# Performance work log

Hardware: AMD Instinct MI355X
Metric: run time of the kernel (lower is better)

## Reference

```python
import jax, jax.numpy as jnp
import numpy as np

B, S, D = 2, 1024, 768      # batch, seq, d_model
F, F_UP = 8192, 8192        # downstream / upstream dictionary sizes
K = 64                      # top-k of the downstream AE
MASK_DENSITY = 0.05         # fraction of allowed feature-feature connections


def setup_inputs() -> dict:
    key = jax.random.key(0)
    ks = jax.random.split(key, 12)
    inv_sqrt_d = 1.0 / np.sqrt(D)
    resid = jax.random.normal(ks[0], (B, S, D), dtype=jnp.float32)
    # upstream pruned features: k-sparse-ish non-negative activations
    pruned0 = jax.nn.relu(jax.random.normal(ks[1], (B, S, F_UP)) - 2.0).astype(jnp.float32)
    pruned1 = jax.nn.relu(jax.random.normal(ks[2], (B, S, F_UP)) - 2.0).astype(jnp.float32)
    feature_buffer = jnp.zeros((B, S, F), dtype=jnp.float32)
    W_enc = jax.random.normal(ks[3], (F, D), dtype=jnp.float32) * inv_sqrt_d
    b_enc = jax.random.normal(ks[4], (F,), dtype=jnp.float32) * 0.01
    W_dec = jax.random.normal(ks[5], (F, D), dtype=jnp.float32) * inv_sqrt_d
    b_dec = jax.random.normal(ks[6], (D,), dtype=jnp.float32) * 0.01
    W_dec_up0 = jax.random.normal(ks[7], (F_UP, D), dtype=jnp.float32) * inv_sqrt_d
    W_dec_up1 = jax.random.normal(ks[8], (F_UP, D), dtype=jnp.float32) * inv_sqrt_d
    b_dec_up0 = jax.random.normal(ks[9], (D,), dtype=jnp.float32) * 0.01
    b_dec_up1 = jax.random.normal(ks[10], (D,), dtype=jnp.float32) * 0.01
    km0, km1 = jax.random.split(ks[11])
    mask0 = (jax.random.uniform(km0, (F, F_UP)) < MASK_DENSITY).astype(jnp.float32)
    mask1 = (jax.random.uniform(km1, (F, F_UP)) < MASK_DENSITY).astype(jnp.float32)
    return {
        "resid": resid, "pruned0": pruned0, "pruned1": pruned1,
        "feature_buffer": feature_buffer,
        "W_enc": W_enc, "b_enc": b_enc, "W_dec": W_dec, "b_dec": b_dec,
        "W_dec_up0": W_dec_up0, "W_dec_up1": W_dec_up1,
        "b_dec_up0": b_dec_up0, "b_dec_up1": b_dec_up1,
        "mask0": mask0, "mask1": mask1, "k": K,
    }


def reference(resid, pruned0, pruned1, feature_buffer,
              W_enc, b_enc, W_dec, b_dec,
              W_dec_up0, W_dec_up1, b_dec_up0, b_dec_up1,
              mask0, mask1, k):
    # initial contributions: encode the cached residual stream, [B,S,F]
    approx = jnp.einsum("bsd,fd->bsf", resid, W_enc)
    upstream_bias = b_dec_up0 + b_dec_up1
    # accumulate connection-masked upstream contributions
    for pruned, W_dec_up, mask in ((pruned0, W_dec_up0, mask0),
                                   (pruned1, W_dec_up1, mask1)):
        # masked virtual weights: [F, F_up]
        virtual = jnp.einsum("fd,ud->fu", W_enc, W_dec_up) * mask
        approx = approx + jnp.einsum("bsu,fu->bsf", pruned, virtual)
    # bias correction: project summed upstream decoder biases, add encoder bias
    approx = approx + jnp.einsum("fd,d->f", W_enc, upstream_bias) + b_enc
    # topk (unsorted set equals torch's sorted=False), relu, scatter into buffer
    top_vals, top_idx = jax.lax.top_k(approx, k)        # [B,S,k]
    top_vals = jax.nn.relu(top_vals)
    Bn, Sn, Fn = feature_buffer.shape
    bi = jnp.arange(Bn)[:, None, None]
    si = jnp.arange(Sn)[None, :, None]
    feat_buffer = jnp.zeros_like(feature_buffer).at[bi, si, top_idx].set(top_vals)
    # dense decode
    reconstructions = jnp.einsum("bsf,fd->bsd", feat_buffer, W_dec) + b_dec
    return feat_buffer, reconstructions
```

## Files before the change

kernel.cpp:

```cpp
#include <hip/hip_runtime.h>
#include <stdint.h>

typedef unsigned long long u64;
typedef unsigned int u32;
typedef unsigned short u16;

#define F_DIM 8192
#define U_DIM 8192
#define D_DIM 768
#define NTOK  2048
#define KSEL  64
#define ROWCAP 544
#define TILE  256
#define NFT   32
#define NUT   32
#define DCH   32
#define ENTCAP 3840
#define NBIN  1024
#define TT    128
#define NTT   16
#define FT3   64
#define NFB   (F_DIM / FT3)
#define UCH   1024
#define NUCH  (U_DIM / UCH)
#define CCAP  4096
#define LCAP  32768

__global__ void k_bias(const float* __restrict__ Wenc, const float* __restrict__ benc,
                       const float* __restrict__ b0, const float* __restrict__ b1,
                       float* __restrict__ t_bias) {
    int wid = threadIdx.x >> 6, lane = threadIdx.x & 63;
    int f = blockIdx.x * 4 + wid;
    const float* row = Wenc + (size_t)f * D_DIM;
    float s = 0.f;
    for (int j = lane; j < D_DIM; j += 64) s += row[j] * (b0[j] + b1[j]);
    #pragma unroll
    for (int off = 32; off; off >>= 1) s += __shfl_down(s, off, 64);
    if (lane == 0) t_bias[f] = s + benc[f];
}

__global__ void k_mask_scan(const float* __restrict__ mask0, const float* __restrict__ mask1,
                            int* __restrict__ rowcnt_tile, u64* __restrict__ bitmap) {
    __shared__ int rc[TILE][4];
    int ut = blockIdx.x, ft = blockIdx.y, l = blockIdx.z;
    const float* mask = l ? mask1 : mask0;
    int tid = threadIdx.x, lane = tid & 63, wid = tid >> 6;
    int u = ut * TILE + tid;
    int f0 = ft * TILE;
    u64* bm = bitmap + (((size_t)(l * NFT + ft) * NUT + ut) * TILE) * 4;
    for (int fl = 0; fl < TILE; ++fl) {
        float v = mask[(size_t)(f0 + fl) * U_DIM + u];
        u64 bal = __ballot(v != 0.0f);
        if (lane == 0) { bm[(size_t)fl * 4 + wid] = bal; rc[fl][wid] = __popcll(bal); }
    }
    __syncthreads();
    rowcnt_tile[(size_t)(l * NUT + ut) * F_DIM + f0 + tid] =
        rc[tid][0] + rc[tid][1] + rc[tid][2] + rc[tid][3];
}

__global__ void k_row_prefix(const int* __restrict__ rowcnt_tile, int* __restrict__ base_r,
                             int* __restrict__ rowcnt_tot) {
    int idx = blockIdx.x * blockDim.x + threadIdx.x;
    int l = idx >> 13, f = idx & (F_DIM - 1);
    int run = 0;
    for (int ut = 0; ut < NUT; ++ut) {
        int c = rowcnt_tile[(size_t)(l * NUT + ut) * F_DIM + f];
        base_r[(size_t)(l * NUT + ut) * F_DIM + f] = run;
        run += c;
    }
    rowcnt_tot[l * F_DIM + f] = run < ROWCAP ? run : ROWCAP;
}

__global__ __launch_bounds__(256, 2) void k_virt_build(
        const float* __restrict__ Wenc, const float* __restrict__ Wup0,
        const float* __restrict__ Wup1, const u64* __restrict__ bitmap,
        const int* __restrict__ base_r, u16* __restrict__ csr_u, float* __restrict__ csr_v) {
    __shared__ u64 bm[TILE][4];
    __shared__ int cs[TILE];
    __shared__ unsigned char entu[ENTCAP];
    __shared__ float acc[ENTCAP];
    __shared__ float wu_t[DCH][TILE + 1];
    int ut = blockIdx.x, ft = blockIdx.y, l = blockIdx.z;
    const float* Wup = l ? Wup1 : Wup0;
    int tid = threadIdx.x;
    int u0 = ut * TILE, f0 = ft * TILE;

    const u64* gbm = bitmap + (((size_t)(l * NFT + ft) * NUT + ut) * TILE) * 4;
    for (int i = tid; i < TILE * 4; i += 256) ((u64*)bm)[i] = gbm[i];
    __syncthreads();

    int cnt = 0;
    #pragma unroll
    for (int w = 0; w < 4; ++w) cnt += (int)__popcll(bm[tid][w]);
    cs[tid] = cnt;
    __syncthreads();
    for (int off = 1; off < 256; off <<= 1) {
        int v = (tid >= off) ? cs[tid - off] : 0;
        __syncthreads();
        cs[tid] += v;
        __syncthreads();
    }
    int cstart = cs[tid] - cnt;
    {
        int i = 0;
        #pragma unroll
        for (int w = 0; w < 4; ++w) {
            u64 word = bm[tid][w];
            while (word) {
                int b = __builtin_ctzll(word); word &= word - 1;
                int p = cstart + i;
                if (p < ENTCAP) entu[p] = (unsigned char)(w * 64 + b);
                ++i;
            }
        }
    }
    for (int i = tid; i < ENTCAP; i += 256) acc[i] = 0.f;
    __syncthreads();

    float we[DCH];
    for (int d0 = 0; d0 < D_DIM; d0 += DCH) {
        const float* ur = Wup + (size_t)(u0 + tid) * D_DIM + d0;
        #pragma unroll
        for (int j = 0; j < DCH; j += 4) {
            float4 t4 = *(const float4*)(ur + j);
            wu_t[j][tid] = t4.x; wu_t[j + 1][tid] = t4.y;
            wu_t[j + 2][tid] = t4.z; wu_t[j + 3][tid] = t4.w;
        }
        const float* wr = Wenc + (size_t)(f0 + tid) * D_DIM + d0;
        #pragma unroll
        for (int j = 0; j < DCH; j += 4) {
            float4 t4 = *(const float4*)(wr + j);
            we[j] = t4.x; we[j + 1] = t4.y; we[j + 2] = t4.z; we[j + 3] = t4.w;
        }
        __syncthreads();
        for (int i = 0; i < cnt; ++i) {
            int p = cstart + i;
            if (p >= ENTCAP) break;
            int ul = entu[p];
            float s = 0.f;
            #pragma unroll
            for (int j = 0; j < DCH; ++j) s += we[j] * wu_t[j][ul];
            acc[p] += s;
        }
        __syncthreads();
    }
    int f = f0 + tid;
    int bse = base_r[(size_t)(l * NUT + ut) * F_DIM + f];
    size_t rb = ((size_t)l * F_DIM + f) * ROWCAP;
    for (int i = 0; i < cnt; ++i) {
        int p = cstart + i;
        if (p >= ENTCAP) break;
        int slot = bse + i;
        if (slot < ROWCAP) {
            csr_u[rb + slot] = (u16)(u0 + entu[p]);
            csr_v[rb + slot] = acc[p];
        }
    }
}

__global__ void k_zero(int* __restrict__ p, int n) {
    int i = (blockIdx.x * blockDim.x + threadIdx.x) * 4;
    if (i < n) *(int4*)(p + i) = make_int4(0, 0, 0, 0);
}

__global__ __launch_bounds__(256) void k_ptok_count(
        const float* __restrict__ pruned0, const float* __restrict__ pruned1,
        int* __restrict__ cnt_g) {
    int t = blockIdx.x, l = blockIdx.y;
    int tt = t >> 7;
    const float* Pr = (l ? pruned1 : pruned0) + (size_t)t * U_DIM;
    int* cg = cnt_g + (size_t)(l * NTT + tt) * U_DIM;
    int tid = threadIdx.x;
    #pragma unroll
    for (int it = 0; it < U_DIM / 1024; ++it) {
        int u0 = it * 1024 + tid * 4;
        float4 v4 = *(const float4*)(Pr + u0);
        float vv[4] = {v4.x, v4.y, v4.z, v4.w};
        #pragma unroll
        for (int j = 0; j < 4; ++j)
            if (vv[j] != 0.0f) atomicAdd(&cg[u0 + j], 1);
    }
}

__global__ __launch_bounds__(256) void k_ptok_scan(
        const int* __restrict__ cnt_g, u32* __restrict__ off_u, int* __restrict__ tot_cnt) {
    __shared__ u32 part[256];
    int ltt = blockIdx.x;
    const int* cg = cnt_g + (size_t)ltt * U_DIM;
    u32* ou = off_u + (size_t)ltt * U_DIM;
    int tid = threadIdx.x;
    int b0 = tid * 32;
    u32 s = 0;
    for (int j = 0; j < 32; ++j) s += (u32)cg[b0 + j];
    part[tid] = s;
    __syncthreads();
    for (int off = 1; off < 256; off <<= 1) {
        u32 v = (tid >= off) ? part[tid - off] : 0;
        __syncthreads();
        part[tid] += v;
        __syncthreads();
    }
    u32 run = part[tid] - s;
    for (int j = 0; j < 32; ++j) { ou[b0 + j] = run; run += (u32)cg[b0 + j]; }
    if (tid == 255) tot_cnt[ltt] = (int)run;
}

__global__ __launch_bounds__(256) void k_ptok_fill(
        const float* __restrict__ pruned0, const float* __restrict__ pruned1,
        int* __restrict__ cnt_g, const u32* __restrict__ off_u,
        u64* __restrict__ lists_c) {
    int t = blockIdx.x, l = blockIdx.y;
    int tt = t >> 7, tl = t & (TT - 1);
    const float* Pr = (l ? pruned1 : pruned0) + (size_t)t * U_DIM;
    int ltt = l * NTT + tt;
    int* cg = cnt_g + (size_t)ltt * U_DIM;
    const u32* ou = off_u + (size_t)ltt * U_DIM;
    u64* Lc = lists_c + (size_t)ltt * LCAP;
    int tid = threadIdx.x;
    #pragma unroll
    for (int it = 0; it < U_DIM / 1024; ++it) {
        int u0 = it * 1024 + tid * 4;
        float4 v4 = *(const float4*)(Pr + u0);
        float vv[4] = {v4.x, v4.y, v4.z, v4.w};
        #pragma unroll
        for (int j = 0; j < 4; ++j) {
            float v = vv[j];
            if (v != 0.0f) {
                int u = u0 + j;
                int a = atomicSub(&cg[u], 1) - 1;
                u32 slot = ou[u] + (u32)a;
                if (slot < (u32)LCAP)
                    Lc[slot] = ((u64)__float_as_uint(v) << 32) | (unsigned)tl;
            }
        }
    }
}

__global__ __launch_bounds__(512, 4) void k_contrib3(
        const u16* __restrict__ csr_u, const float* __restrict__ csr_v,
        const int* __restrict__ base_r, const int* __restrict__ rowcnt_tot,
        const u32* __restrict__ off_u, const int* __restrict__ tot_cnt,
        const u64* __restrict__ lists_c, float* __restrict__ C) {
    __shared__ float accum[TT][FT3 + 1];
    __shared__ u32 soff[UCH + 1];
    __shared__ u64 cbuf[CCAP];
    int raw = blockIdx.x;
    int xcd = raw & 7, idx = raw >> 3;
    int ft = idx & (NFB - 1);
    int tth = idx >> 7;
    int tt = xcd + 8 * tth;
    int tid = threadIdx.x, lane = tid & 63, wid = tid >> 6;
    for (int i = tid; i < TT * (FT3 + 1); i += 512) ((float*)accum)[i] = 0.f;
    for (int l = 0; l < 2; ++l) {
        int ltt = l * NTT + tt;
        const u32* offs = off_u + (size_t)ltt * U_DIM;
        const u64* Lc = lists_c + (size_t)ltt * LCAP;
        for (int uc = 0; uc < NUCH; ++uc) {
            __syncthreads();
            int ub = uc * UCH;
            for (int i = tid; i < UCH + 1; i += 512) {
                int u = ub + i;
                soff[i] = (u < U_DIM) ? offs[u] : (u32)tot_cnt[ltt];
            }
            __syncthreads();
            u32 cbase = soff[0];
            int scount = (int)(soff[UCH] - cbase);
            if (scount > CCAP) scount = CCAP;
            for (int i = tid; i < scount; i += 512) cbuf[i] = Lc[cbase + i];
            __syncthreads();
            int ut0 = uc * (UCH / TILE);
            #pragma unroll
            for (int rr = 0; rr < FT3 / 8; ++rr) {
                int r = wid * 8 + rr;
                int f = ft * FT3 + r;
                int tot = rowcnt_tot[l * F_DIM + f];
                int s0 = base_r[(size_t)(l * NUT + ut0) * F_DIM + f];
                int s1 = (ut0 + 4 < NUT) ? base_r[(size_t)(l * NUT + ut0 + 4) * F_DIM + f]
                                         : 0x7fffffff;
                if (s0 > tot) s0 = tot;
                if (s1 > tot) s1 = tot;
                size_t rb = ((size_t)l * F_DIM + f) * ROWCAP;
                for (int e = s0 + lane; e < s1; e += 64) {
                    int u = csr_u[rb + e];
                    float v = csr_v[rb + e];
                    int ul = u - ub;
                    u32 o0 = soff[ul] - cbase;
                    u32 o1 = soff[ul + 1] - cbase;
                    if (o1 > (u32)CCAP) o1 = (u32)CCAP;
                    for (u32 j = o0; j < o1; ++j) {
                        u64 pk = cbuf[j];
                        int tok = (int)(unsigned)pk;
                        float p = __uint_as_float((unsigned)(pk >> 32));
                        atomicAdd(&accum[tok][r], p * v);
                    }
                }
            }
        }
    }
    __syncthreads();
    int t0 = tt * TT, f0 = ft * FT3;
    for (int i = tid; i < TT * FT3; i += 512) {
        int tok = i >> 6, r = i & (FT3 - 1);
        C[(size_t)(t0 + tok) * F_DIM + f0 + r] = accum[tok][r];
    }
}

#define BM 128
#define BN 128
#define BK 16
__global__ __launch_bounds__(256) void k_encoder(
        const float* __restrict__ resid, const float* __restrict__ Wenc,
        const float* __restrict__ t_bias, float* __restrict__ C) {
    __shared__ float As[BK][BM + 4];
    __shared__ float Bs[BK][BN + 4];
    int tid = threadIdx.x;
    int m0 = blockIdx.y * BM, n0 = blockIdx.x * BN;
    int mt = tid & 15, nt = tid >> 4;
    float acc[8][8] = {};
    for (int k0 = 0; k0 < D_DIM; k0 += BK) {
        if (tid < 128) {
            const float* ar = resid + (size_t)(m0 + tid) * D_DIM + k0;
            #pragma unroll
            for (int j = 0; j < BK; j += 4) {
                float4 t4 = *(const float4*)(ar + j);
                As[j][tid] = t4.x; As[j + 1][tid] = t4.y;
                As[j + 2][tid] = t4.z; As[j + 3][tid] = t4.w;
            }
        } else {
            int r = tid - 128;
            const float* br = Wenc + (size_t)(n0 + r) * D_DIM + k0;
            #pragma unroll
            for (int j = 0; j < BK; j += 4) {
                float4 t4 = *(const float4*)(br + j);
                Bs[j][r] = t4.x; Bs[j + 1][r] = t4.y;
                Bs[j + 2][r] = t4.z; Bs[j + 3][r] = t4.w;
            }
        }
        __syncthreads();
        #pragma unroll
        for (int k = 0; k < BK; ++k) {
            float a[8], bb[8];
            *(float4*)&a[0]  = *(const float4*)&As[k][mt * 8];
            *(float4*)&a[4]  = *(const float4*)&As[k][mt * 8 + 4];
            *(float4*)&bb[0] = *(const float4*)&Bs[k][nt * 8];
            *(float4*)&bb[4] = *(const float4*)&Bs[k][nt * 8 + 4];
            #pragma unroll
            for (int i = 0; i < 8; ++i)
                #pragma unroll
                for (int j = 0; j < 8; ++j) acc[i][j] += a[i] * bb[j];
        }
        __syncthreads();
    }
    float tb[8];
    #pragma unroll
    for (int j = 0; j < 8; ++j) tb[j] = t_bias[n0 + nt * 8 + j];
    #pragma unroll
    for (int i = 0; i < 8; ++i) {
        float* cr = C + (size_t)(m0 + mt * 8 + i) * F_DIM + n0 + nt * 8;
        #pragma unroll
        for (int j = 0; j < 8; ++j) cr[j] += acc[i][j] + tb[j];
    }
}

__global__ __launch_bounds__(256) void k_select(
        float* __restrict__ C, int* __restrict__ sel_idx, float* __restrict__ sel_val) {
    __shared__ float row[F_DIM];
    __shared__ int hist[NBIN];
    __shared__ int bstar, nsure, ncand;
    __shared__ float sure_v[64];  __shared__ int sure_f[64];
    __shared__ float cand_v[256]; __shared__ int cand_f[256];
    __shared__ float out_v[KSEL]; __shared__ int out_f[KSEL];
    int t = blockIdx.x, tid = threadIdx.x;
    float* Crow = C + (size_t)t * F_DIM;
    for (int i = tid; i < F_DIM; i += 256) row[i] = Crow[i];
    for (int i = tid; i < NBIN; i += 256) hist[i] = 0;
    __syncthreads();
    for (int i = tid; i < F_DIM; i += 256) {
        int b = (int)floorf((row[i] + 16.0f) * 32.0f);
        b = b < 0 ? 0 : (b > NBIN - 1 ? NBIN - 1 : b);
        atomicAdd(&hist[b], 1);
    }
    __syncthreads();
    if (tid == 0) {
        int cum = 0, bs = 0;
        for (int b = NBIN - 1; b >= 0; --b) { cum += hist[b]; if (cum >= KSEL) { bs = b; break; } }
        bstar = bs; nsure = 0; ncand = 0;
    }
    __syncthreads();
    int bs = bstar;
    for (int i = tid; i < F_DIM; i += 256) {
        float v = row[i];
        int b = (int)floorf((v + 16.0f) * 32.0f);
        b = b < 0 ? 0 : (b > NBIN - 1 ? NBIN - 1 : b);
        if (b > bs) {
            int p = atomicAdd(&nsure, 1);
            if (p < 64) { sure_v[p] = v; sure_f[p] = i; }
        } else if (b == bs) {
            int p = atomicAdd(&ncand, 1);
            if (p < 256) { cand_v[p] = v; cand_f[p] = i; }
        }
    }
    __syncthreads();
    if (tid == 0) {
        int c1 = nsure; if (c1 > KSEL) c1 = KSEL;
        for (int i = 0; i < c1; ++i) { out_v[i] = sure_v[i]; out_f[i] = sure_f[i]; }
        int need = KSEL - c1;
        int nc = ncand; if (nc > 256) nc = 256;
        for (int s = 0; s < need; ++s) {
            float bv = -1e30f; int bf = 0x7fffffff, bi = -1;
            for (int i = 0; i < nc; ++i) {
                float v = cand_v[i];
                if (v > bv || (v == bv && cand_f[i] < bf)) { bv = v; bf = cand_f[i]; bi = i; }
            }
            if (bi < 0) { out_v[c1 + s] = 0.f; out_f[c1 + s] = 0; continue; }
            out_v[c1 + s] = cand_v[bi]; out_f[c1 + s] = cand_f[bi];
            cand_v[bi] = -1e30f;
        }
    }
    __syncthreads();
    for (int i = tid; i < F_DIM; i += 256) Crow[i] = 0.0f;
    __syncthreads();
    if (tid < KSEL) {
        float v = out_v[tid]; int f = out_f[tid];
        float rv = v > 0.f ? v : 0.f;
        Crow[f] = rv;
        sel_idx[t * KSEL + tid] = f;
        sel_val[t * KSEL + tid] = rv;
    }
}

__global__ __launch_bounds__(256) void k_decode(
        const int* __restrict__ sel_idx, const float* __restrict__ sel_val,
        const float* __restrict__ Wdec, const float* __restrict__ bdec,
        float* __restrict__ recon) {
    __shared__ int sf[KSEL]; __shared__ float sv[KSEL];
    int t = blockIdx.x, tid = threadIdx.x;
    if (tid < KSEL) { sf[tid] = sel_idx[t * KSEL + tid]; sv[tid] = sel_val[t * KSEL + tid]; }
    __syncthreads();
    for (int d = tid; d < D_DIM; d += 256) {
        float s = bdec[d];
        #pragma unroll 8
        for (int j = 0; j < KSEL; ++j) s += sv[j] * Wdec[(size_t)sf[j] * D_DIM + d];
        recon[(size_t)t * D_DIM + d] = s;
    }
}

extern "C" void kernel_launch(void* const* d_in, const int* in_sizes, int n_in,
                              void* d_out, int out_size, void* d_ws, size_t ws_size,
                              hipStream_t stream) {
    (void)in_sizes; (void)n_in; (void)out_size; (void)ws_size;
    const float* resid   = (const float*)d_in[0];
    const float* pruned0 = (const float*)d_in[1];
    const float* pruned1 = (const float*)d_in[2];
    const float* Wenc    = (const float*)d_in[4];
    const float* benc    = (const float*)d_in[5];
    const float* Wdec    = (const float*)d_in[6];
    const float* bdec    = (const float*)d_in[7];
    const float* Wup0    = (const float*)d_in[8];
    const float* Wup1    = (const float*)d_in[9];
    const float* bup0    = (const float*)d_in[10];
    const float* bup1    = (const float*)d_in[11];
    const float* mask0   = (const float*)d_in[12];
    const float* mask1   = (const float*)d_in[13];

    char* ws = (char*)d_ws;
    size_t o = 0;
    auto alloc = [&](size_t bytes) -> char* {
        o = (o + 255) & ~(size_t)255;
        char* p = ws + o; o += bytes; return p;
    };
    float* t_bias      = (float*)alloc((size_t)F_DIM * 4);
    int*   rowcnt_tile = (int*)  alloc((size_t)2 * NUT * F_DIM * 4);
    int*   base_r      = (int*)  alloc((size_t)2 * NUT * F_DIM * 4);
    int*   rowcnt_tot  = (int*)  alloc((size_t)2 * F_DIM * 4);
    u64*   bitmap      = (u64*)  alloc((size_t)2 * NFT * NUT * TILE * 4 * 8);
    u16*   csr_u       = (u16*)  alloc((size_t)2 * F_DIM * ROWCAP * 2);
    float* csr_v       = (float*)alloc((size_t)2 * F_DIM * ROWCAP * 4);
    u32*   off_u       = (u32*)  alloc((size_t)2 * NTT * U_DIM * 4);
    int*   tot_cnt     = (int*)  alloc((size_t)2 * NTT * 4);
    u64*   lists_c     = (u64*)  alloc((size_t)2 * NTT * LCAP * 8);
    int*   cnt_g       = (int*)  alloc((size_t)2 * NTT * U_DIM * 4);
    int*   sel_idx     = (int*)  alloc((size_t)NTOK * KSEL * 4);
    float* sel_val     = (float*)alloc((size_t)NTOK * KSEL * 4);

    float* out   = (float*)d_out;
    float* C     = out;
    float* recon = out + (size_t)NTOK * F_DIM;

    const int NCNT = 2 * NTT * U_DIM;

    hipLaunchKernelGGL(k_bias,       dim3(F_DIM / 4),        dim3(256), 0, stream,
                       Wenc, benc, bup0, bup1, t_bias);
    hipLaunchKernelGGL(k_mask_scan,  dim3(NUT, NFT, 2),      dim3(256), 0, stream,
                       mask0, mask1, rowcnt_tile, bitmap);
    hipLaunchKernelGGL(k_row_prefix, dim3(2 * F_DIM / 256),  dim3(256), 0, stream,
                       rowcnt_tile, base_r, rowcnt_tot);
    hipLaunchKernelGGL(k_zero,       dim3(NCNT / 1024),      dim3(256), 0, stream,
                       cnt_g, NCNT);
    hipLaunchKernelGGL(k_virt_build, dim3(NUT, NFT, 2),      dim3(256), 0, stream,
                       Wenc, Wup0, Wup1, bitmap, base_r, csr_u, csr_v);
    hipLaunchKernelGGL(k_ptok_count, dim3(NTOK, 2),          dim3(256), 0, stream,
                       pruned0, pruned1, cnt_g);
    hipLaunchKernelGGL(k_ptok_scan,  dim3(2 * NTT),          dim3(256), 0, stream,
                       cnt_g, off_u, tot_cnt);
    hipLaunchKernelGGL(k_ptok_fill,  dim3(NTOK, 2),          dim3(256), 0, stream,
                       pruned0, pruned1, cnt_g, off_u, lists_c);
    hipLaunchKernelGGL(k_contrib3,   dim3(NFB * NTT),        dim3(512), 0, stream,
                       csr_u, csr_v, base_r, rowcnt_tot, off_u, tot_cnt, lists_c, C);
    hipLaunchKernelGGL(k_encoder,    dim3(F_DIM / BN, NTOK / BM), dim3(256), 0, stream,
                       resid, Wenc, t_bias, C);
    hipLaunchKernelGGL(k_select,     dim3(NTOK),             dim3(256), 0, stream,
                       C, sel_idx, sel_val);
    hipLaunchKernelGGL(k_decode,     dim3(NTOK),             dim3(256), 0, stream,
                       sel_idx, sel_val, Wdec, bdec, recon);
}
```

Baseline: 4.611 ms.

## Replace token-tiled contribution kernel with global per-feature sparse lists

```diff
diff --git a/kernel.cpp b/kernel.cpp
--- a/kernel.cpp
+++ b/kernel.cpp
@@ -17,14 +17,8 @@
 #define DCH   32
 #define ENTCAP 3840
 #define NBIN  1024
-#define TT    128
-#define NTT   16
-#define FT3   64
-#define NFB   (F_DIM / FT3)
-#define UCH   1024
-#define NUCH  (U_DIM / UCH)
-#define CCAP  4096
-#define LCAP  32768
+#define LCAPG (1 << 19)
+#define OFFP  8200
 
 __global__ void k_bias(const float* __restrict__ Wenc, const float* __restrict__ benc,
                        const float* __restrict__ b0, const float* __restrict__ b1,
@@ -167,9 +161,8 @@
         const float* __restrict__ pruned0, const float* __restrict__ pruned1,
         int* __restrict__ cnt_g) {
     int t = blockIdx.x, l = blockIdx.y;
-    int tt = t >> 7;
     const float* Pr = (l ? pruned1 : pruned0) + (size_t)t * U_DIM;
-    int* cg = cnt_g + (size_t)(l * NTT + tt) * U_DIM;
+    int* cg = cnt_g + (size_t)l * U_DIM;
     int tid = threadIdx.x;
     #pragma unroll
     for (int it = 0; it < U_DIM / 1024; ++it) {
@@ -183,11 +176,11 @@
 }
 
 __global__ __launch_bounds__(256) void k_ptok_scan(
-        const int* __restrict__ cnt_g, u32* __restrict__ off_u, int* __restrict__ tot_cnt) {
+        const int* __restrict__ cnt_g, u32* __restrict__ off_g) {
     __shared__ u32 part[256];
-    int ltt = blockIdx.x;
-    const int* cg = cnt_g + (size_t)ltt * U_DIM;
-    u32* ou = off_u + (size_t)ltt * U_DIM;
+    int l = blockIdx.x;
+    const int* cg = cnt_g + (size_t)l * U_DIM;
+    u32* ou = off_g + (size_t)l * OFFP;
     int tid = threadIdx.x;
     int b0 = tid * 32;
     u32 s = 0;
@@ -202,20 +195,18 @@
     }
     u32 run = part[tid] - s;
     for (int j = 0; j < 32; ++j) { ou[b0 + j] = run; run += (u32)cg[b0 + j]; }
-    if (tid == 255) tot_cnt[ltt] = (int)run;
+    if (tid == 255) ou[U_DIM] = run;
 }
 
 __global__ __launch_bounds__(256) void k_ptok_fill(
         const float* __restrict__ pruned0, const float* __restrict__ pruned1,
-        int* __restrict__ cnt_g, const u32* __restrict__ off_u,
-        u64* __restrict__ lists_c) {
+        int* __restrict__ cnt_g, const u32* __restrict__ off_g,
+        u64* __restrict__ lists_g) {
     int t = blockIdx.x, l = blockIdx.y;
-    int tt = t >> 7, tl = t & (TT - 1);
     const float* Pr = (l ? pruned1 : pruned0) + (size_t)t * U_DIM;
-    int ltt = l * NTT + tt;
-    int* cg = cnt_g + (size_t)ltt * U_DIM;
-    const u32* ou = off_u + (size_t)ltt * U_DIM;
-    u64* Lc = lists_c + (size_t)ltt * LCAP;
+    int* cg = cnt_g + (size_t)l * U_DIM;
+    const u32* ou = off_g + (size_t)l * OFFP;
+    u64* Lg = lists_g + (size_t)l * LCAPG;
     int tid = threadIdx.x;
     #pragma unroll
     for (int it = 0; it < U_DIM / 1024; ++it) {
@@ -229,79 +220,76 @@
                 int u = u0 + j;
                 int a = atomicSub(&cg[u], 1) - 1;
                 u32 slot = ou[u] + (u32)a;
-                if (slot < (u32)LCAP)
-                    Lc[slot] = ((u64)__float_as_uint(v) << 32) | (unsigned)tl;
-            }
-        }
-    }
-}
-
-__global__ __launch_bounds__(512, 4) void k_contrib3(
+                if (slot < (u32)LCAPG)
+                    Lg[slot] = ((u64)__float_as_uint(v) << 32) | (unsigned)t;
+            }
+        }
+    }
+}
+
+__global__ __launch_bounds__(512, 2) void k_contrib4(
         const u16* __restrict__ csr_u, const float* __restrict__ csr_v,
-        const int* __restrict__ base_r, const int* __restrict__ rowcnt_tot,
-        const u32* __restrict__ off_u, const int* __restrict__ tot_cnt,
-        const u64* __restrict__ lists_c, float* __restrict__ C) {
-    __shared__ float accum[TT][FT3 + 1];
-    __shared__ u32 soff[UCH + 1];
-    __shared__ u64 cbuf[CCAP];
-    int raw = blockIdx.x;
-    int xcd = raw & 7, idx = raw >> 3;
-    int ft = idx & (NFB - 1);
-    int tth = idx >> 7;
-    int tt = xcd + 8 * tth;
+        const int* __restrict__ rowcnt_tot, const u32* __restrict__ off_g,
+        const u64* __restrict__ lists_g, float* __restrict__ C) {
+    __shared__ float accum[8][NTOK];
+    __shared__ u64 se_uv[8][64];
+    __shared__ u64 se_off[8][64];
+    int fb = blockIdx.x;
     int tid = threadIdx.x, lane = tid & 63, wid = tid >> 6;
-    for (int i = tid; i < TT * (FT3 + 1); i += 512) ((float*)accum)[i] = 0.f;
+    for (int i = tid; i < 8 * NTOK; i += 512) ((float*)accum)[i] = 0.f;
+    __syncthreads();
+    int f = fb * 8 + wid;
     for (int l = 0; l < 2; ++l) {
-        int ltt = l * NTT + tt;
-        const u32* offs = off_u + (size_t)ltt * U_DIM;
-        const u64* Lc = lists_c + (size_t)ltt * LCAP;
-        for (int uc = 0; uc < NUCH; ++uc) {
-            __syncthreads();
-            int ub = uc * UCH;
-            for (int i = tid; i < UCH + 1; i += 512) {
-                int u = ub + i;
-                soff[i] = (u < U_DIM) ? offs[u] : (u32)tot_cnt[ltt];
-            }
-            __syncthreads();
-            u32 cbase = soff[0];
-            int scount = (int)(soff[UCH] - cbase);
-            if (scount > CCAP) scount = CCAP;
-            for (int i = tid; i < scount; i += 512) cbuf[i] = Lc[cbase + i];
-            __syncthreads();
-            int ut0 = uc * (UCH / TILE);
-            #pragma unroll
-            for (int rr = 0; rr < FT3 / 8; ++rr) {
-                int r = wid * 8 + rr;
-                int f = ft * FT3 + r;
-                int tot = rowcnt_tot[l * F_DIM + f];
-                int s0 = base_r[(size_t)(l * NUT + ut0) * F_DIM + f];
-                int s1 = (ut0 + 4 < NUT) ? base_r[(size_t)(l * NUT + ut0 + 4) * F_DIM + f]
-                                         : 0x7fffffff;
-                if (s0 > tot) s0 = tot;
-                if (s1 > tot) s1 = tot;
-                size_t rb = ((size_t)l * F_DIM + f) * ROWCAP;
-                for (int e = s0 + lane; e < s1; e += 64) {
-                    int u = csr_u[rb + e];
-                    float v = csr_v[rb + e];
-                    int ul = u - ub;
-                    u32 o0 = soff[ul] - cbase;
-                    u32 o1 = soff[ul + 1] - cbase;
-                    if (o1 > (u32)CCAP) o1 = (u32)CCAP;
-                    for (u32 j = o0; j < o1; ++j) {
-                        u64 pk = cbuf[j];
-                        int tok = (int)(unsigned)pk;
-                        float p = __uint_as_float((unsigned)(pk >> 32));
-                        atomicAdd(&accum[tok][r], p * v);
-                    }
+        int cnt = rowcnt_tot[l * F_DIM + f];
+        size_t rb = ((size_t)l * F_DIM + f) * ROWCAP;
+        const u32* OF = off_g + (size_t)l * OFFP;
+        const u64* Lg = lists_g + (size_t)l * LCAPG;
+        for (int eb = 0; eb < cnt; eb += 64) {
+            int n = cnt - eb; if (n > 64) n = 64;
+            if (lane < n) {
+                int u = csr_u[rb + eb + lane];
+                float v = csr_v[rb + eb + lane];
+                u32 o0 = OF[u], o1 = OF[u + 1];
+                if (o1 > (u32)LCAPG) o1 = (u32)LCAPG;
+                if (o0 > o1) o0 = o1;
+                se_uv[wid][lane] = ((u64)__float_as_uint(v) << 32) | (u32)u;
+                se_off[wid][lane] = ((u64)o1 << 32) | o0;
+            }
+            u64 so = se_off[wid][0];
+            u32 co0 = (u32)so, co1 = (u32)(so >> 32);
+            u64 pk = (co0 + lane < co1) ? Lg[co0 + (u32)lane] : 0;
+            for (int e = 0; e < n; ++e) {
+                u32 o0 = co0, o1 = co1;
+                u64 mypk = pk;
+                if (e + 1 < n) {
+                    u64 so2 = se_off[wid][e + 1];
+                    co0 = (u32)so2; co1 = (u32)(so2 >> 32);
+                    pk = (co0 + lane < co1) ? Lg[co0 + (u32)lane] : 0;
                 }
-            }
-        }
-    }
-    __syncthreads();
-    int t0 = tt * TT, f0 = ft * FT3;
-    for (int i = tid; i < TT * FT3; i += 512) {
-        int tok = i >> 6, r = i & (FT3 - 1);
-        C[(size_t)(t0 + tok) * F_DIM + f0 + r] = accum[tok][r];
+                float v = __uint_as_float((u32)(se_uv[wid][e] >> 32));
+                if (o0 + lane < o1) {
+                    int tok = (int)((u32)mypk & 2047u);
+                    float p = __uint_as_float((u32)(mypk >> 32));
+                    atomicAdd(&accum[wid][tok], p * v);
+                }
+                for (u32 j = o0 + 64 + lane; j < o1; j += 64) {
+                    u64 pk2 = Lg[j];
+                    int tok = (int)((u32)pk2 & 2047u);
+                    float p = __uint_as_float((u32)(pk2 >> 32));
+                    atomicAdd(&accum[wid][tok], p * v);
+                }
+            }
+        }
+    }
+    __syncthreads();
+    int f0 = fb * 8;
+    for (int tok = tid; tok < NTOK; tok += 512) {
+        float4 a, b;
+        a.x = accum[0][tok]; a.y = accum[1][tok]; a.z = accum[2][tok]; a.w = accum[3][tok];
+        b.x = accum[4][tok]; b.y = accum[5][tok]; b.z = accum[6][tok]; b.w = accum[7][tok];
+        float* cp = C + (size_t)tok * F_DIM + f0;
+        *(float4*)cp = a;
+        *(float4*)(cp + 4) = b;
     }
 }
 
@@ -476,10 +464,9 @@
     u64*   bitmap      = (u64*)  alloc((size_t)2 * NFT * NUT * TILE * 4 * 8);
     u16*   csr_u       = (u16*)  alloc((size_t)2 * F_DIM * ROWCAP * 2);
     float* csr_v       = (float*)alloc((size_t)2 * F_DIM * ROWCAP * 4);
-    u32*   off_u       = (u32*)  alloc((size_t)2 * NTT * U_DIM * 4);
-    int*   tot_cnt     = (int*)  alloc((size_t)2 * NTT * 4);
-    u64*   lists_c     = (u64*)  alloc((size_t)2 * NTT * LCAP * 8);
-    int*   cnt_g       = (int*)  alloc((size_t)2 * NTT * U_DIM * 4);
+    u32*   off_g       = (u32*)  alloc((size_t)2 * OFFP * 4);
+    u64*   lists_g     = (u64*)  alloc((size_t)2 * LCAPG * 8);
+    int*   cnt_g       = (int*)  alloc((size_t)2 * U_DIM * 4);
     int*   sel_idx     = (int*)  alloc((size_t)NTOK * KSEL * 4);
     float* sel_val     = (float*)alloc((size_t)NTOK * KSEL * 4);
 
@@ -487,7 +474,7 @@
     float* C     = out;
     float* recon = out + (size_t)NTOK * F_DIM;
 
-    const int NCNT = 2 * NTT * U_DIM;
+    const int NCNT = 2 * U_DIM;
 
     hipLaunchKernelGGL(k_bias,       dim3(F_DIM / 4),        dim3(256), 0, stream,
                        Wenc, benc, bup0, bup1, t_bias);
@@ -501,12 +488,12 @@
                        Wenc, Wup0, Wup1, bitmap, base_r, csr_u, csr_v);
     hipLaunchKernelGGL(k_ptok_count, dim3(NTOK, 2),          dim3(256), 0, stream,
                        pruned0, pruned1, cnt_g);
-    hipLaunchKernelGGL(k_ptok_scan,  dim3(2 * NTT),          dim3(256), 0, stream,
-                       cnt_g, off_u, tot_cnt);
+    hipLaunchKernelGGL(k_ptok_scan,  dim3(2),                dim3(256), 0, stream,
+                       cnt_g, off_g);
     hipLaunchKernelGGL(k_ptok_fill,  dim3(NTOK, 2),          dim3(256), 0, stream,
-                       pruned0, pruned1, cnt_g, off_u, lists_c);
-    hipLaunchKernelGGL(k_contrib3,   dim3(NFB * NTT),        dim3(512), 0, stream,
-                       csr_u, csr_v, base_r, rowcnt_tot, off_u, tot_cnt, lists_c, C);
+                       pruned0, pruned1, cnt_g, off_g, lists_g);
+    hipLaunchKernelGGL(k_contrib4,   dim3(F_DIM / 8),        dim3(512), 0, stream,
+                       csr_u, csr_v, rowcnt_tot, off_g, lists_g, C);
     hipLaunchKernelGGL(k_encoder,    dim3(F_DIM / BN, NTOK / BM), dim3(256), 0, stream,
                        resid, Wenc, t_bias, C);
     hipLaunchKernelGGL(k_select,     dim3(NTOK),             dim3(256), 0, stream,
```

New measurement: 4.468 ms. -3.1%, faster.
